# Optimization experiments

Hardware: AMD Instinct MI355X
Metric: run time of the kernel (lower is better)

Reference implementation:

```python
import jax, jax.numpy as jnp
import numpy as np

N = 8192
IN_FEATURES = 512
OUT_FEATURES = 256
ALPHA = 0.2  # LeakyReLU negative slope
MASK_VAL = -1e11


def setup_inputs() -> dict:
    key = jax.random.key(0)
    k_h, k_adj, k_w, k_a1, k_a2 = jax.random.split(key, 5)
    h = jax.random.normal(k_h, (N, IN_FEATURES), dtype=jnp.float32)
    adj = jax.random.randint(k_adj, (N, N), 0, 2, dtype=jnp.int32)
    # xavier_uniform with gain=1.414 for Linear weight [out, in]
    def xavier(k, fan_out, fan_in, gain=1.414):
        bound = gain * np.sqrt(6.0 / (fan_in + fan_out))
        return jax.random.uniform(k, (fan_out, fan_in), dtype=jnp.float32,
                                  minval=-bound, maxval=bound)
    W = xavier(k_w, OUT_FEATURES, IN_FEATURES)          # linear_w.weight
    a1 = xavier(k_a1, 1, OUT_FEATURES)[0]               # linear_a_1.weight -> [out]
    a2 = xavier(k_a2, 1, OUT_FEATURES)[0]               # linear_a_2.weight -> [out]
    return {"h": h, "W": W, "a1": a1, "a2": a2, "adj": adj}


def reference(h, W, a1, a2, adj):
    # wh: [N, F_out]
    wh = jnp.einsum("ni,oi->no", h, W)
    wh1 = wh @ a1  # [N]
    wh2 = wh @ a2  # [N]
    # additive attention scores e_ij = leakyrelu(wh1_i + wh2_j): [N, N]
    e = jax.nn.leaky_relu(wh1[:, None] + wh2[None, :], negative_slope=ALPHA)
    scores = jnp.where(adj > 0, e, MASK_VAL)
    attention = jax.nn.softmax(scores, axis=-1)  # dropout p=0 -> identity
    h_new = attention @ wh  # [N, F_out]
    return jax.nn.elu(h_new)  # concat=True path
```

## Files before the change

### kernel.cpp

```cpp
#include <hip/hip_runtime.h>


typedef __attribute__((ext_vector_type(8))) short short8;
typedef __attribute__((ext_vector_type(4))) float f32x4;

__device__ __forceinline__ unsigned short f2bf(float f) {
  unsigned int u = __float_as_uint(f);
  unsigned int r = u + 0x7FFFu + ((u >> 16) & 1u);
  return (unsigned short)(r >> 16);
}

__global__ __launch_bounds__(512) void k_u(const float* __restrict__ W,
                                           const float* __restrict__ a1,
                                           const float* __restrict__ a2,
                                           float* __restrict__ u1,
                                           float* __restrict__ u2) {
  __shared__ float p1[16][32], p2[16][32];
  const int tid = threadIdx.x;
  const int kk = tid & 31, og = tid >> 5;
  const int k0 = blockIdx.x * 32;
  float s1 = 0.f, s2 = 0.f;
#pragma unroll
  for (int j = 0; j < 16; j++) {
    const int o = og * 16 + j;
    const float w = W[(size_t)o * 512 + k0 + kk];
    s1 += w * a1[o];
    s2 += w * a2[o];
  }
  p1[og][kk] = s1;
  p2[og][kk] = s2;
  __syncthreads();
  if (tid < 32) {
    float t1 = 0.f, t2 = 0.f;
#pragma unroll
    for (int g = 0; g < 16; g++) { t1 += p1[g][tid]; t2 += p2[g][tid]; }
    u1[k0 + tid] = t1;
    u2[k0 + tid] = t2;
  }
}

__global__ __launch_bounds__(256) void k_rowvec(const float* __restrict__ h,
                                                const float* __restrict__ u1,
                                                const float* __restrict__ u2,
                                                float* __restrict__ wh1,
                                                float* __restrict__ wh2,
                                                float* __restrict__ pmax) {
  __shared__ float su1[512], su2[512];
  __shared__ float smax[4];
  const int tid = threadIdx.x;
  for (int i = tid; i < 512; i += 256) { su1[i] = u1[i]; su2[i] = u2[i]; }
  __syncthreads();
  const int lane = tid & 63;
  const int row = blockIdx.x * 4 + (tid >> 6);
  const float* hp = h + (size_t)row * 512 + lane * 8;
  float4 x0 = *(const float4*)hp;
  float4 x1 = *(const float4*)(hp + 4);
  const float* q1 = su1 + lane * 8;
  const float* q2 = su2 + lane * 8;
  float s1 = x0.x * q1[0] + x0.y * q1[1] + x0.z * q1[2] + x0.w * q1[3]
           + x1.x * q1[4] + x1.y * q1[5] + x1.z * q1[6] + x1.w * q1[7];
  float s2 = x0.x * q2[0] + x0.y * q2[1] + x0.z * q2[2] + x0.w * q2[3]
           + x1.x * q2[4] + x1.y * q2[5] + x1.z * q2[6] + x1.w * q2[7];
#pragma unroll
  for (int off = 32; off >= 1; off >>= 1) {
    s1 += __shfl_xor(s1, off);
    s2 += __shfl_xor(s2, off);
  }
  if (lane == 0) {
    wh1[row] = s1;
    wh2[row] = s2;
    smax[tid >> 6] = s2;
  }
  __syncthreads();
  if (tid == 0)
    pmax[blockIdx.x] = fmaxf(fmaxf(smax[0], smax[1]), fmaxf(smax[2], smax[3]));
}

__global__ __launch_bounds__(256) void k_max(const float* __restrict__ pmax,
                                             float* __restrict__ gmax) {
  __shared__ float sm[4];
  const int tid = threadIdx.x;
  float m = -3.0e38f;
  for (int i = tid; i < 2048; i += 256) m = fmaxf(m, pmax[i]);
#pragma unroll
  for (int off = 32; off >= 1; off >>= 1) m = fmaxf(m, __shfl_xor(m, off));
  if ((tid & 63) == 0) sm[tid >> 6] = m;
  __syncthreads();
  if (tid == 0) gmax[0] = fmaxf(fmaxf(sm[0], sm[1]), fmaxf(sm[2], sm[3]));
}

__global__ __launch_bounds__(512, 1) void k_wh(const float* __restrict__ h,
                                               const float* __restrict__ W,
                                               unsigned short* __restrict__ whT) {
  __shared__ uint4 lds[2560];
  const int tid = threadIdx.x;
  const int i0 = blockIdx.x * 64;
  const int lane = tid & 63, wid = tid >> 6;
  const int wm = wid >> 2, wn = wid & 3;
  const int l16 = lane & 15, lq = lane >> 4;
  const int hr = tid >> 3, hc = tid & 7;
  const int wr = tid >> 1, wc = tid & 1;

  f32x4 acc[2][4] = {};

  for (int t = 0; t < 8; t++) {
    const int k0 = t * 64;
    const float* hp = h + (size_t)(i0 + hr) * 512 + k0 + hc * 8;
    float4 hx = *(const float4*)hp;
    float4 hy = *(const float4*)(hp + 4);
    const float* wp = W + (size_t)wr * 512 + k0 + wc * 32;
    float4 wv[8];
#pragma unroll
    for (int q = 0; q < 8; q++) wv[q] = *(const float4*)(wp + q * 4);

    __syncthreads();
    uint4 hw;
    hw.x = (unsigned)f2bf(hx.x) | ((unsigned)f2bf(hx.y) << 16);
    hw.y = (unsigned)f2bf(hx.z) | ((unsigned)f2bf(hx.w) << 16);
    hw.z = (unsigned)f2bf(hy.x) | ((unsigned)f2bf(hy.y) << 16);
    hw.w = (unsigned)f2bf(hy.z) | ((unsigned)f2bf(hy.w) << 16);
    lds[hr * 8 + (hc ^ (hr & 7))] = hw;
#pragma unroll
    for (int q = 0; q < 4; q++) {
      uint4 ww;
      ww.x = (unsigned)f2bf(wv[2 * q].x) | ((unsigned)f2bf(wv[2 * q].y) << 16);
      ww.y = (unsigned)f2bf(wv[2 * q].z) | ((unsigned)f2bf(wv[2 * q].w) << 16);
      ww.z = (unsigned)f2bf(wv[2 * q + 1].x) | ((unsigned)f2bf(wv[2 * q + 1].y) << 16);
      ww.w = (unsigned)f2bf(wv[2 * q + 1].z) | ((unsigned)f2bf(wv[2 * q + 1].w) << 16);
      lds[512 + wr * 8 + ((wc * 4 + q) ^ (wr & 7))] = ww;
    }
    __syncthreads();
#pragma unroll
    for (int ks = 0; ks < 2; ks++) {
      const int r0 = wm * 32 + l16, r1 = r0 + 16;
      short8 fa0 = *(const short8*)&lds[r0 * 8 + ((ks * 4 + lq) ^ (r0 & 7))];
      short8 fa1 = *(const short8*)&lds[r1 * 8 + ((ks * 4 + lq) ^ (r1 & 7))];
#pragma unroll
      for (int fn = 0; fn < 4; fn++) {
        const int bn = wn * 64 + fn * 16 + l16;
        short8 fb = *(const short8*)&lds[512 + bn * 8 + ((ks * 4 + lq) ^ (bn & 7))];
        acc[0][fn] = __builtin_amdgcn_mfma_f32_16x16x32_bf16(fa0, fb, acc[0][fn], 0, 0, 0);
        acc[1][fn] = __builtin_amdgcn_mfma_f32_16x16x32_bf16(fa1, fb, acc[1][fn], 0, 0, 0);
      }
    }
  }
#pragma unroll
  for (int fm = 0; fm < 2; fm++) {
#pragma unroll
    for (int fn = 0; fn < 4; fn++) {
      const int n = wn * 64 + fn * 16 + l16;
      const int m0 = i0 + wm * 32 + fm * 16 + lq * 4;
      uint2 o;
      o.x = (unsigned)f2bf(acc[fm][fn][0]) | ((unsigned)f2bf(acc[fm][fn][1]) << 16);
      o.y = (unsigned)f2bf(acc[fm][fn][2]) | ((unsigned)f2bf(acc[fm][fn][3]) << 16);
      *(uint2*)(whT + (size_t)n * 8192 + m0) = o;
    }
  }
}

struct PFR {
  int4 a0, a1, a2, a3;
  float4 z0, z1, z2, z3;
};

__global__ __launch_bounds__(512, 2) void k_attn(
    const int* __restrict__ adj, const unsigned short* __restrict__ whT,
    const float* __restrict__ wh1, const float* __restrict__ wh2,
    const float* __restrict__ gmax,
    float* __restrict__ out0, float* __restrict__ out1,
    float* __restrict__ out2, float* __restrict__ out3,
    float* __restrict__ denp) {
  __shared__ uint4 lds_t[3 * 2048];
  const int NT = 32;
  const int tid = threadIdx.x;
  const int bid = blockIdx.x;
  const int sb = (bid & 7) >> 1;
  const int mb = ((bid >> 3) << 1) | (bid & 1);
  const int i0 = mb * 128;
  const int jbase = sb * 2048;
  const int lane = tid & 63, w = tid >> 6;
  const int l16 = lane & 15, q = lane >> 4;
  const int row_a = i0 + w * 16 + l16;

  const float wh2max = gmax[0];
  const float wh1r = wh1[row_a];
  const float tm = wh1r + wh2max;
  const float Mi = tm > 0.f ? tm : 0.2f * tm;

  const int* adjp = adj + (size_t)row_a * 8192 + jbase + q * 8;
  const float* wh2p = wh2 + jbase + q * 8;

  f32x4 acc[16] = {};
  float dsum = 0.f;
  short8 pa0, pa1;
  PFR PA, PB;

#define STAGE(TT, SLOT)                                                        \
  do {                                                                         \
    const int tt_ = ((TT) < NT) ? (TT) : 0;                                    \
    const size_t gj_ = (size_t)(jbase + tt_ * 64);                             \
    _Pragma("unroll") for (int qq = 0; qq < 4; qq++) {                         \
      const int L = qq * 512 + tid;                                            \
      const int row = L >> 3, sub = L & 7;                                     \
      const int boff = (sub * 16) ^ ((row & 7) << 4);                          \
      const char* src_ =                                                       \
          (const char*)(whT + (size_t)row * 8192 + gj_) + boff;                \
      char* dst_ = (char*)lds_t + (SLOT) * 32768 + L * 16;                     \
      __builtin_amdgcn_global_load_lds(                                        \
          (const __attribute__((address_space(1))) unsigned int*)src_,         \
          (__attribute__((address_space(3))) unsigned int*)dst_, 16, 0, 0);    \
    }                                                                          \
  } while (0)

#define PFLOAD(R, T)                                    \
  do {                                                  \
    const int o_ = (((T) < NT) ? (T) : 0) * 64;         \
    R.a0 = *(const int4*)(adjp + o_);                   \
    R.a1 = *(const int4*)(adjp + o_ + 4);               \
    R.a2 = *(const int4*)(adjp + o_ + 32);              \
    R.a3 = *(const int4*)(adjp + o_ + 36);              \
    R.z0 = *(const float4*)(wh2p + o_);                 \
    R.z1 = *(const float4*)(wh2p + o_ + 4);             \
    R.z2 = *(const float4*)(wh2p + o_ + 32);            \
    R.z3 = *(const float4*)(wh2p + o_ + 36);            \
  } while (0)

#define COMPUTE(R)                                                             \
  do {                                                                         \
    int av[16] = {R.a0.x, R.a0.y, R.a0.z, R.a0.w, R.a1.x, R.a1.y, R.a1.z,      \
                  R.a1.w, R.a2.x, R.a2.y, R.a2.z, R.a2.w, R.a3.x, R.a3.y,      \
                  R.a3.z, R.a3.w};                                             \
    float zv[16] = {R.z0.x, R.z0.y, R.z0.z, R.z0.w, R.z1.x, R.z1.y, R.z1.z,    \
                    R.z1.w, R.z2.x, R.z2.y, R.z2.z, R.z2.w, R.z3.x, R.z3.y,    \
                    R.z3.z, R.z3.w};                                           \
    float pv[16];                                                              \
    _Pragma("unroll") for (int i = 0; i < 16; i++) {                           \
      float x = wh1r + zv[i];                                                  \
      float e = x > 0.f ? x : 0.2f * x;                                        \
      float p = (av[i] > 0) ? __expf(e - Mi) : 0.f;                            \
      pv[i] = p;                                                               \
      dsum += p;                                                               \
    }                                                                          \
    _Pragma("unroll") for (int i = 0; i < 8; i++) {                            \
      pa0[i] = (short)f2bf(pv[i]);                                             \
      pa1[i] = (short)f2bf(pv[8 + i]);                                         \
    }                                                                          \
  } while (0)

#define FENCE_BAR                                        \
  do {                                                   \
    asm volatile("s_waitcnt vmcnt(12)" ::: "memory");    \
    __builtin_amdgcn_s_barrier();                        \
  } while (0)

#define MFMAPH(SLOT)                                                           \
  do {                                                                         \
    const char* lb_ = (const char*)lds_t + (SLOT) * 32768;                     \
    _Pragma("unroll") for (int nb = 0; nb < 16; nb++) {                        \
      const int n_ = nb * 16 + l16;                                            \
      const int rb_ = n_ * 128;                                                \
      const int sw_ = (n_ & 7) << 4;                                           \
      short8 fb0 = *(const short8*)(lb_ + rb_ + ((q * 16) ^ sw_));             \
      short8 fb1 = *(const short8*)(lb_ + rb_ + ((64 + q * 16) ^ sw_));        \
      acc[nb] = __builtin_amdgcn_mfma_f32_16x16x32_bf16(pa0, fb0, acc[nb], 0, 0, 0); \
      acc[nb] = __builtin_amdgcn_mfma_f32_16x16x32_bf16(pa1, fb1, acc[nb], 0, 0, 0); \
    }                                                                          \
  } while (0)

  STAGE(0, 0);
  STAGE(1, 1);
  PFLOAD(PA, 0);

  int sA = 0, sB = 1, sC = 2;
  for (int t = 0; t < NT; t += 2) {
    PFLOAD(PB, t + 1);
    COMPUTE(PA);
    FENCE_BAR;
    STAGE(t + 2, sC);
    MFMAPH(sA);
    PFLOAD(PA, t + 2);
    COMPUTE(PB);
    FENCE_BAR;
    STAGE(t + 3, sA);
    MFMAPH(sB);
    int tmp = sA; sA = sC; sC = sB; sB = tmp;
  }

#undef STAGE
#undef PFLOAD
#undef COMPUTE
#undef FENCE_BAR
#undef MFMAPH

  float* outp = (sb == 0) ? out0 : (sb == 1) ? out1 : (sb == 2) ? out2 : out3;
  const int r0 = i0 + w * 16 + q * 4;
#pragma unroll
  for (int nb = 0; nb < 16; nb++) {
    const int col = nb * 16 + l16;
#pragma unroll
    for (int r = 0; r < 4; r++)
      outp[(size_t)(r0 + r) * 256 + col] = acc[nb][r];
  }

  dsum += __shfl_xor(dsum, 16);
  dsum += __shfl_xor(dsum, 32);
  if (lane < 16) denp[sb * 8192 + i0 + w * 16 + lane] = dsum;
}

__global__ __launch_bounds__(256) void k_out(float* __restrict__ out,
                                             const float* __restrict__ p1,
                                             const float* __restrict__ p2,
                                             const float* __restrict__ p3,
                                             const float* __restrict__ denp) {
  const int idx = blockIdx.x * 256 + threadIdx.x;
  const int row = idx >> 6;
  float4 o = ((const float4*)out)[idx];
  float4 a = ((const float4*)p1)[idx];
  float4 b = ((const float4*)p2)[idx];
  float4 c = ((const float4*)p3)[idx];
  const float inv =
      1.0f / (denp[row] + denp[8192 + row] + denp[16384 + row] + denp[24576 + row]);
  float v0 = (o.x + a.x + b.x + c.x) * inv;
  float v1 = (o.y + a.y + b.y + c.y) * inv;
  float v2 = (o.z + a.z + b.z + c.z) * inv;
  float v3 = (o.w + a.w + b.w + c.w) * inv;
  v0 = v0 > 0.f ? v0 : expm1f(v0);
  v1 = v1 > 0.f ? v1 : expm1f(v1);
  v2 = v2 > 0.f ? v2 : expm1f(v2);
  v3 = v3 > 0.f ? v3 : expm1f(v3);
  ((float4*)out)[idx] = make_float4(v0, v1, v2, v3);
}

extern "C" void kernel_launch(void* const* d_in, const int* in_sizes, int n_in,
                              void* d_out, int out_size, void* d_ws, size_t ws_size,
                              hipStream_t stream) {
  const float* h = (const float*)d_in[0];
  const float* W = (const float*)d_in[1];
  const float* a1 = (const float*)d_in[2];
  const float* a2 = (const float*)d_in[3];
  const int* adj = (const int*)d_in[4];
  float* out = (float*)d_out;
  char* ws = (char*)d_ws;

  unsigned short* whT = (unsigned short*)ws;
  float* part1 = (float*)(ws + (4u << 20));
  float* part2 = (float*)(ws + (12u << 20));
  float* part3 = (float*)(ws + (20u << 20));
  float* denp = (float*)(ws + (28u << 20));
  float* wh1 = denp + 4 * 8192;
  float* wh2 = wh1 + 8192;
  float* pmax = wh2 + 8192;
  float* u1 = pmax + 2048;
  float* u2 = u1 + 512;
  float* gmax = u2 + 512;

  hipLaunchKernelGGL(k_u, dim3(16), dim3(512), 0, stream, W, a1, a2, u1, u2);
  hipLaunchKernelGGL(k_rowvec, dim3(2048), dim3(256), 0, stream, h, u1, u2, wh1,
                     wh2, pmax);
  hipLaunchKernelGGL(k_max, dim3(1), dim3(256), 0, stream, pmax, gmax);
  hipLaunchKernelGGL(k_wh, dim3(128), dim3(512), 0, stream, h, W, whT);
  hipLaunchKernelGGL(k_attn, dim3(256), dim3(512), 0, stream, adj, whT, wh1,
                     wh2, gmax, out, part1, part2, part3, denp);
  hipLaunchKernelGGL(k_out, dim3(2048), dim3(256), 0, stream, out, part1, part2,
                     part3, denp);
  (void)in_sizes; (void)n_in; (void)out_size; (void)ws_size;
}
```

Measured before the change: 145.9 us.

## Restructure attention kernel into 2-wave blocks with doubled row tiles and exp2 softmax

The attention kernel moves from 512-thread blocks to 128-thread blocks, with each wave handling 32 rows (two 16-row MFMA tiles) so every B-fragment read from LDS feeds twice as many MFMAs. The staging ring shrinks from three slots to two, and wh2 is cached in LDS instead of being reloaded from global memory. Scores are pre-scaled by log2(e) so exp2 with folded constants replaces expf. The global-max reduction kernel is folded into block 0 of k_wh to save a launch. In exchange, register pressure goes up with doubled accumulators, there are only 2 waves per block, and the two-slot ring leaves less room to overlap loads with MFMA.

```diff
diff --git a/kernel.cpp b/kernel.cpp
--- a/kernel.cpp
+++ b/kernel.cpp
@@ -3,6 +3,8 @@
 
 typedef __attribute__((ext_vector_type(8))) short short8;
 typedef __attribute__((ext_vector_type(4))) float f32x4;
+
+#define LOG2E 1.4426950408889634f
 
 __device__ __forceinline__ unsigned short f2bf(float f) {
   unsigned int u = __float_as_uint(f);
@@ -67,33 +69,37 @@
     s2 += __shfl_xor(s2, off);
   }
   if (lane == 0) {
-    wh1[row] = s1;
-    wh2[row] = s2;
-    smax[tid >> 6] = s2;
+    wh1[row] = s1 * LOG2E;
+    wh2[row] = s2 * LOG2E;
+    smax[tid >> 6] = s2 * LOG2E;
   }
   __syncthreads();
   if (tid == 0)
     pmax[blockIdx.x] = fmaxf(fmaxf(smax[0], smax[1]), fmaxf(smax[2], smax[3]));
 }
 
-__global__ __launch_bounds__(256) void k_max(const float* __restrict__ pmax,
-                                             float* __restrict__ gmax) {
-  __shared__ float sm[4];
-  const int tid = threadIdx.x;
-  float m = -3.0e38f;
-  for (int i = tid; i < 2048; i += 256) m = fmaxf(m, pmax[i]);
-#pragma unroll
-  for (int off = 32; off >= 1; off >>= 1) m = fmaxf(m, __shfl_xor(m, off));
-  if ((tid & 63) == 0) sm[tid >> 6] = m;
-  __syncthreads();
-  if (tid == 0) gmax[0] = fmaxf(fmaxf(sm[0], sm[1]), fmaxf(sm[2], sm[3]));
-}
-
 __global__ __launch_bounds__(512, 1) void k_wh(const float* __restrict__ h,
                                                const float* __restrict__ W,
-                                               unsigned short* __restrict__ whT) {
+                                               unsigned short* __restrict__ whT,
+                                               const float* __restrict__ pmax,
+                                               float* __restrict__ gmax) {
   __shared__ uint4 lds[2560];
+  __shared__ float sred[8];
   const int tid = threadIdx.x;
+  if (blockIdx.x == 0) {
+    float m = -3.0e38f;
+    for (int i = tid; i < 2048; i += 512) m = fmaxf(m, pmax[i]);
+#pragma unroll
+    for (int off = 32; off >= 1; off >>= 1) m = fmaxf(m, __shfl_xor(m, off));
+    if ((tid & 63) == 0) sred[tid >> 6] = m;
+    __syncthreads();
+    if (tid == 0) {
+      float g = sred[0];
+#pragma unroll
+      for (int i = 1; i < 8; i++) g = fmaxf(g, sred[i]);
+      gmax[0] = g;
+    }
+  }
   const int i0 = blockIdx.x * 64;
   const int lane = tid & 63, wid = tid >> 6;
   const int wm = wid >> 2, wn = wid & 3;
@@ -159,152 +165,176 @@
 }
 
 struct PFR {
-  int4 a0, a1, a2, a3;
-  float4 z0, z1, z2, z3;
+  int4 l0, l1, l2, l3, h0, h1, h2, h3;
 };
 
-__global__ __launch_bounds__(512, 2) void k_attn(
+__global__ __launch_bounds__(128, 1) void k_attn(
     const int* __restrict__ adj, const unsigned short* __restrict__ whT,
-    const float* __restrict__ wh1, const float* __restrict__ wh2,
+    const float* __restrict__ wh1v, const float* __restrict__ wh2v,
     const float* __restrict__ gmax,
     float* __restrict__ out0, float* __restrict__ out1,
     float* __restrict__ out2, float* __restrict__ out3,
     float* __restrict__ denp) {
-  __shared__ uint4 lds_t[3 * 2048];
+  __shared__ uint4 ring[2][2048];
+  __shared__ float wh2s[2048];
   const int NT = 32;
   const int tid = threadIdx.x;
   const int bid = blockIdx.x;
   const int sb = (bid & 7) >> 1;
   const int mb = ((bid >> 3) << 1) | (bid & 1);
-  const int i0 = mb * 128;
+  const int i0 = mb * 64;
   const int jbase = sb * 2048;
   const int lane = tid & 63, w = tid >> 6;
   const int l16 = lane & 15, q = lane >> 4;
-  const int row_a = i0 + w * 16 + l16;
-
-  const float wh2max = gmax[0];
-  const float wh1r = wh1[row_a];
-  const float tm = wh1r + wh2max;
-  const float Mi = tm > 0.f ? tm : 0.2f * tm;
-
-  const int* adjp = adj + (size_t)row_a * 8192 + jbase + q * 8;
-  const float* wh2p = wh2 + jbase + q * 8;
-
-  f32x4 acc[16] = {};
-  float dsum = 0.f;
-  short8 pa0, pa1;
+  const int row_lo = i0 + w * 32 + l16;
+
+  for (int i = tid; i < 512; i += 128)
+    ((float4*)wh2s)[i] = ((const float4*)(wh2v + jbase))[i];
+
+  const float M2 = gmax[0];
+  const float w1lo = wh1v[row_lo];
+  const float w1hi = wh1v[row_lo + 16];
+  float tv = w1lo + M2;
+  const float Milo = tv > 0.f ? tv : 0.2f * tv;
+  tv = w1hi + M2;
+  const float Mihi = tv > 0.f ? tv : 0.2f * tv;
+  const float c1lo = w1lo - Milo, c2lo = 0.2f * w1lo - Milo;
+  const float c1hi = w1hi - Mihi, c2hi = 0.2f * w1hi - Mihi;
+
+  const int* ap_lo = adj + (size_t)row_lo * 8192 + jbase + q * 8;
+  const int* ap_hi = ap_lo + 16 * 8192;
+
+  f32x4 accL[16] = {}, accH[16] = {};
+  float dsL = 0.f, dsH = 0.f;
+  short8 paL0, paL1, paH0, paH1;
   PFR PA, PB;
+
+#define PFLOAD(R, T)                              \
+  do {                                            \
+    const int o_ = (((T) < NT) ? (T) : 0) * 64;   \
+    R.l0 = *(const int4*)(ap_lo + o_);            \
+    R.l1 = *(const int4*)(ap_lo + o_ + 4);        \
+    R.l2 = *(const int4*)(ap_lo + o_ + 32);       \
+    R.l3 = *(const int4*)(ap_lo + o_ + 36);       \
+    R.h0 = *(const int4*)(ap_hi + o_);            \
+    R.h1 = *(const int4*)(ap_hi + o_ + 4);        \
+    R.h2 = *(const int4*)(ap_hi + o_ + 32);       \
+    R.h3 = *(const int4*)(ap_hi + o_ + 36);       \
+  } while (0)
+
+#define COMPUTE(R, T)                                                          \
+  do {                                                                         \
+    const int o_ = (((T) < NT) ? (T) : 0) * 64 + q * 8;                        \
+    float4 z0 = *(const float4*)(wh2s + o_);                                   \
+    float4 z1 = *(const float4*)(wh2s + o_ + 4);                               \
+    float4 z2 = *(const float4*)(wh2s + o_ + 32);                              \
+    float4 z3 = *(const float4*)(wh2s + o_ + 36);                              \
+    float zv[16] = {z0.x, z0.y, z0.z, z0.w, z1.x, z1.y, z1.z, z1.w,            \
+                    z2.x, z2.y, z2.z, z2.w, z3.x, z3.y, z3.z, z3.w};           \
+    int al[16] = {R.l0.x, R.l0.y, R.l0.z, R.l0.w, R.l1.x, R.l1.y, R.l1.z,      \
+                  R.l1.w, R.l2.x, R.l2.y, R.l2.z, R.l2.w, R.l3.x, R.l3.y,      \
+                  R.l3.z, R.l3.w};                                             \
+    int ah[16] = {R.h0.x, R.h0.y, R.h0.z, R.h0.w, R.h1.x, R.h1.y, R.h1.z,      \
+                  R.h1.w, R.h2.x, R.h2.y, R.h2.z, R.h2.w, R.h3.x, R.h3.y,      \
+                  R.h3.z, R.h3.w};                                             \
+    float pl[16], ph[16];                                                      \
+    _Pragma("unroll") for (int i = 0; i < 16; i++) {                           \
+      float e1 = fmaxf(c1lo + zv[i], __builtin_fmaf(0.2f, zv[i], c2lo));       \
+      float p = (al[i] > 0) ? __builtin_amdgcn_exp2f(e1) : 0.f;                \
+      pl[i] = p;                                                               \
+      dsL += p;                                                                \
+      float e2 = fmaxf(c1hi + zv[i], __builtin_fmaf(0.2f, zv[i], c2hi));       \
+      p = (ah[i] > 0) ? __builtin_amdgcn_exp2f(e2) : 0.f;                      \
+      ph[i] = p;                                                               \
+      dsH += p;                                                                \
+    }                                                                          \
+    _Pragma("unroll") for (int i = 0; i < 8; i++) {                            \
+      paL0[i] = (short)f2bf(pl[i]);                                            \
+      paL1[i] = (short)f2bf(pl[8 + i]);                                        \
+      paH0[i] = (short)f2bf(ph[i]);                                            \
+      paH1[i] = (short)f2bf(ph[8 + i]);                                        \
+    }                                                                          \
+  } while (0)
 
 #define STAGE(TT, SLOT)                                                        \
   do {                                                                         \
     const int tt_ = ((TT) < NT) ? (TT) : 0;                                    \
     const size_t gj_ = (size_t)(jbase + tt_ * 64);                             \
-    _Pragma("unroll") for (int qq = 0; qq < 4; qq++) {                         \
-      const int L = qq * 512 + tid;                                            \
+    _Pragma("unroll") for (int kq = 0; kq < 16; kq++) {                        \
+      const int L = kq * 128 + tid;                                            \
       const int row = L >> 3, sub = L & 7;                                     \
       const int boff = (sub * 16) ^ ((row & 7) << 4);                          \
-      const char* src_ =                                                       \
-          (const char*)(whT + (size_t)row * 8192 + gj_) + boff;                \
-      char* dst_ = (char*)lds_t + (SLOT) * 32768 + L * 16;                     \
+      const char* src_ = (const char*)(whT + (size_t)row * 8192 + gj_) + boff; \
+      char* dst_ = (char*)ring[SLOT] + L * 16;                                 \
       __builtin_amdgcn_global_load_lds(                                        \
           (const __attribute__((address_space(1))) unsigned int*)src_,         \
           (__attribute__((address_space(3))) unsigned int*)dst_, 16, 0, 0);    \
     }                                                                          \
   } while (0)
 
-#define PFLOAD(R, T)                                    \
-  do {                                                  \
-    const int o_ = (((T) < NT) ? (T) : 0) * 64;         \
-    R.a0 = *(const int4*)(adjp + o_);                   \
-    R.a1 = *(const int4*)(adjp + o_ + 4);               \
-    R.a2 = *(const int4*)(adjp + o_ + 32);              \
-    R.a3 = *(const int4*)(adjp + o_ + 36);              \
-    R.z0 = *(const float4*)(wh2p + o_);                 \
-    R.z1 = *(const float4*)(wh2p + o_ + 4);             \
-    R.z2 = *(const float4*)(wh2p + o_ + 32);            \
-    R.z3 = *(const float4*)(wh2p + o_ + 36);            \
-  } while (0)
-
-#define COMPUTE(R)                                                             \
-  do {                                                                         \
-    int av[16] = {R.a0.x, R.a0.y, R.a0.z, R.a0.w, R.a1.x, R.a1.y, R.a1.z,      \
-                  R.a1.w, R.a2.x, R.a2.y, R.a2.z, R.a2.w, R.a3.x, R.a3.y,      \
-                  R.a3.z, R.a3.w};                                             \
-    float zv[16] = {R.z0.x, R.z0.y, R.z0.z, R.z0.w, R.z1.x, R.z1.y, R.z1.z,    \
-                    R.z1.w, R.z2.x, R.z2.y, R.z2.z, R.z2.w, R.z3.x, R.z3.y,    \
-                    R.z3.z, R.z3.w};                                           \
-    float pv[16];                                                              \
-    _Pragma("unroll") for (int i = 0; i < 16; i++) {                           \
-      float x = wh1r + zv[i];                                                  \
-      float e = x > 0.f ? x : 0.2f * x;                                        \
-      float p = (av[i] > 0) ? __expf(e - Mi) : 0.f;                            \
-      pv[i] = p;                                                               \
-      dsum += p;                                                               \
-    }                                                                          \
-    _Pragma("unroll") for (int i = 0; i < 8; i++) {                            \
-      pa0[i] = (short)f2bf(pv[i]);                                             \
-      pa1[i] = (short)f2bf(pv[8 + i]);                                         \
-    }                                                                          \
-  } while (0)
-
-#define FENCE_BAR                                        \
-  do {                                                   \
-    asm volatile("s_waitcnt vmcnt(12)" ::: "memory");    \
-    __builtin_amdgcn_s_barrier();                        \
-  } while (0)
+#define FENCE asm volatile("s_waitcnt vmcnt(8)" ::: "memory")
 
 #define MFMAPH(SLOT)                                                           \
   do {                                                                         \
-    const char* lb_ = (const char*)lds_t + (SLOT) * 32768;                     \
+    const char* lb_ = (const char*)ring[SLOT];                                 \
     _Pragma("unroll") for (int nb = 0; nb < 16; nb++) {                        \
       const int n_ = nb * 16 + l16;                                            \
       const int rb_ = n_ * 128;                                                \
       const int sw_ = (n_ & 7) << 4;                                           \
       short8 fb0 = *(const short8*)(lb_ + rb_ + ((q * 16) ^ sw_));             \
       short8 fb1 = *(const short8*)(lb_ + rb_ + ((64 + q * 16) ^ sw_));        \
-      acc[nb] = __builtin_amdgcn_mfma_f32_16x16x32_bf16(pa0, fb0, acc[nb], 0, 0, 0); \
-      acc[nb] = __builtin_amdgcn_mfma_f32_16x16x32_bf16(pa1, fb1, acc[nb], 0, 0, 0); \
+      accL[nb] = __builtin_amdgcn_mfma_f32_16x16x32_bf16(paL0, fb0, accL[nb], 0, 0, 0); \
+      accL[nb] = __builtin_amdgcn_mfma_f32_16x16x32_bf16(paL1, fb1, accL[nb], 0, 0, 0); \
+      accH[nb] = __builtin_amdgcn_mfma_f32_16x16x32_bf16(paH0, fb0, accH[nb], 0, 0, 0); \
+      accH[nb] = __builtin_amdgcn_mfma_f32_16x16x32_bf16(paH1, fb1, accH[nb], 0, 0, 0); \
     }                                                                          \
   } while (0)
 
+  PFLOAD(PA, 0);
   STAGE(0, 0);
-  STAGE(1, 1);
-  PFLOAD(PA, 0);
-
-  int sA = 0, sB = 1, sC = 2;
+  __syncthreads();
+
   for (int t = 0; t < NT; t += 2) {
     PFLOAD(PB, t + 1);
-    COMPUTE(PA);
-    FENCE_BAR;
-    STAGE(t + 2, sC);
-    MFMAPH(sA);
+    COMPUTE(PA, t);
+    FENCE;
+    __builtin_amdgcn_s_barrier();
+    STAGE(t + 1, 1);
+    MFMAPH(0);
     PFLOAD(PA, t + 2);
-    COMPUTE(PB);
-    FENCE_BAR;
-    STAGE(t + 3, sA);
-    MFMAPH(sB);
-    int tmp = sA; sA = sC; sC = sB; sB = tmp;
-  }
-
-#undef STAGE
+    COMPUTE(PB, t + 1);
+    FENCE;
+    __builtin_amdgcn_s_barrier();
+    STAGE(t + 2, 0);
+    MFMAPH(1);
+  }
+
 #undef PFLOAD
 #undef COMPUTE
-#undef FENCE_BAR
+#undef STAGE
+#undef FENCE
 #undef MFMAPH
 
   float* outp = (sb == 0) ? out0 : (sb == 1) ? out1 : (sb == 2) ? out2 : out3;
-  const int r0 = i0 + w * 16 + q * 4;
+  const int r0 = i0 + w * 32 + q * 4;
 #pragma unroll
   for (int nb = 0; nb < 16; nb++) {
     const int col = nb * 16 + l16;
 #pragma unroll
-    for (int r = 0; r < 4; r++)
-      outp[(size_t)(r0 + r) * 256 + col] = acc[nb][r];
-  }
-
-  dsum += __shfl_xor(dsum, 16);
-  dsum += __shfl_xor(dsum, 32);
-  if (lane < 16) denp[sb * 8192 + i0 + w * 16 + lane] = dsum;
+    for (int r = 0; r < 4; r++) {
+      outp[(size_t)(r0 + r) * 256 + col] = accL[nb][r];
+      outp[(size_t)(r0 + 16 + r) * 256 + col] = accH[nb][r];
+    }
+  }
+
+  dsL += __shfl_xor(dsL, 16);
+  dsL += __shfl_xor(dsL, 32);
+  dsH += __shfl_xor(dsH, 16);
+  dsH += __shfl_xor(dsH, 32);
+  if (lane < 16) {
+    denp[sb * 8192 + i0 + w * 32 + lane] = dsL;
+    denp[sb * 8192 + i0 + w * 32 + 16 + lane] = dsH;
+  }
 }
 
 __global__ __launch_bounds__(256) void k_out(float* __restrict__ out,
@@ -357,9 +387,8 @@
   hipLaunchKernelGGL(k_u, dim3(16), dim3(512), 0, stream, W, a1, a2, u1, u2);
   hipLaunchKernelGGL(k_rowvec, dim3(2048), dim3(256), 0, stream, h, u1, u2, wh1,
                      wh2, pmax);
-  hipLaunchKernelGGL(k_max, dim3(1), dim3(256), 0, stream, pmax, gmax);
-  hipLaunchKernelGGL(k_wh, dim3(128), dim3(512), 0, stream, h, W, whT);
-  hipLaunchKernelGGL(k_attn, dim3(256), dim3(512), 0, stream, adj, whT, wh1,
+  hipLaunchKernelGGL(k_wh, dim3(128), dim3(512), 0, stream, h, W, whT, pmax, gmax);
+  hipLaunchKernelGGL(k_attn, dim3(512), dim3(128), 0, stream, adj, whT, wh1,
                      wh2, gmax, out, part1, part2, part3, denp);
   hipLaunchKernelGGL(k_out, dim3(2048), dim3(256), 0, stream, out, part1, part2,
                      part3, denp);
```

New measurement: 158.0 us. 1.08x slower.
